# Performance work log

Hardware: AMD Instinct MI355X
Metric: run time of the kernel (lower is better)

The kernel has to match this reference:

```python
import jax, jax.numpy as jnp
import numpy as np

EPS = 1e-5  # torch GroupNorm default


def setup_inputs() -> dict:
    key = jax.random.key(0)
    ks = jax.random.split(key, 6)
    C = 256
    B, F, H, W = 1, 8, 32, 32
    scale = 1.0 / np.sqrt(C)  # keep logits well-scaled
    return {
        "x": jax.random.normal(ks[0], (B, C, F, H, W), dtype=jnp.float32),
        "gn_w": jnp.ones((C,), jnp.float32),
        "gn_b": jnp.zeros((C,), jnp.float32),
        "qw": jax.random.normal(ks[1], (C, C), jnp.float32) * scale,
        "qb": jnp.zeros((C,), jnp.float32),
        "kw": jax.random.normal(ks[2], (C, C), jnp.float32) * scale,
        "kb": jnp.zeros((C,), jnp.float32),
        "vw": jax.random.normal(ks[3], (C, C), jnp.float32) * scale,
        "vb": jnp.zeros((C,), jnp.float32),
        "ow": jax.random.normal(ks[4], (C, C), jnp.float32) * scale,
        "ob": jnp.zeros((C,), jnp.float32),
    }


def reference(x, gn_w, gn_b, qw, qb, kw, kb, vw, vb, ow, ob):
    B, C, F, H, W = x.shape
    N = F * H * W
    # GroupNorm(1, C): normalize over (C,F,H,W) per sample, per-channel affine
    mean = jnp.mean(x, axis=(1, 2, 3, 4), keepdims=True)
    var = jnp.var(x, axis=(1, 2, 3, 4), keepdims=True)
    xn = (x - mean) * jax.lax.rsqrt(var + EPS)
    xn = xn * gn_w[None, :, None, None, None] + gn_b[None, :, None, None, None]
    xf = xn.reshape(B, C, N)  # [B, C, N]
    # 1x1x1 Conv3d == channel matmul
    q = jnp.einsum('oc,bcn->bon', qw, xf) + qb[None, :, None]
    k = jnp.einsum('oc,bcn->bon', kw, xf) + kb[None, :, None]
    v = jnp.einsum('oc,bcn->bon', vw, xf) + vb[None, :, None]
    # scores[b, n_q, n_k] = q^T k, scaled by C^-0.5
    scores = jnp.einsum('bcn,bcm->bnm', q, k) * (C ** -0.5)
    weights = jax.nn.softmax(scores, axis=-1)  # over keys
    # attention[b, c, n_q] = sum_m v[b,c,m] * weights[b,n_q,m]
    att = jnp.einsum('bcm,bnm->bcn', v, weights)
    att = jnp.einsum('oc,bcn->bon', ow, att) + ob[None, :, None]
    return xn + att.reshape(B, C, F, H, W)
```

## Files before the change

kernel.cpp:

```cpp
#include <hip/hip_runtime.h>
#include <hip/hip_bf16.h>
#include <cstdint>

#define NSP 8192
#define CCH 256
#define KBLK 32
#define NSPLIT 8
#define KEYS_PER_SPLIT 1024
#define NTILES 32

typedef __attribute__((ext_vector_type(4))) float f32x4;
typedef __attribute__((ext_vector_type(16))) float f32x16;
typedef __attribute__((ext_vector_type(8))) short bf16x8;
typedef __attribute__((ext_vector_type(2))) unsigned int u32x2;

__device__ __forceinline__ ushort f2bf(float f) {
  union { float f; uint32_t u; } v; v.f = f;
  uint32_t r = (v.u + 0x7FFFu + ((v.u >> 16) & 1u)) >> 16;
  return (ushort)r;
}
__device__ __forceinline__ float bf2f(ushort u) {
  union { uint32_t u; float f; } v; v.u = ((uint32_t)u) << 16; return v.f;
}
__device__ __forceinline__ uint32_t pk2bf(float lo, float hi) {
  __hip_bfloat162 h = __float22bfloat162_rn({lo, hi});
  union { __hip_bfloat162 h; uint32_t u; } c; c.h = h; return c.u;
}

__device__ __forceinline__ void gload_lds16(const void* g, void* l) {
  auto gp = (const __attribute__((address_space(1))) uint32_t*)(uintptr_t)g;
  auto lp = (__attribute__((address_space(3))) uint32_t*)(uint32_t)(uintptr_t)l;
  __builtin_amdgcn_global_load_lds(gp, lp, 16, 0, 0);
}

__device__ __forceinline__ void perm32swap(uint32_t& a, uint32_t& b) {
#if __has_builtin(__builtin_amdgcn_permlane32_swap)
  u32x2 r = __builtin_amdgcn_permlane32_swap(a, b, false, false);
  a = r[0]; b = r[1];
#else
  uint32_t sa = __shfl_xor((int)a, 32), sb = __shfl_xor((int)b, 32);
  bool lo = (threadIdx.x & 63) < 32;
  uint32_t na = lo ? a : sb;
  uint32_t nb = lo ? sa : b;
  a = na; b = nb;
#endif
}

__global__ __launch_bounds__(256) void k_stats1(const float* __restrict__ x,
                                                float* __restrict__ part) {
  int t = threadIdx.x, b = blockIdx.x;
  float s = 0.f, ss = 0.f;
  const float4* x4 = (const float4*)x;
  for (int i = 0; i < 4; ++i) {
    float4 v = x4[(size_t)i * 131072 + b * 256 + t];
    s += v.x + v.y + v.z + v.w;
    ss += v.x * v.x + v.y * v.y + v.z * v.z + v.w * v.w;
  }
  for (int m = 1; m < 64; m <<= 1) { s += __shfl_xor(s, m); ss += __shfl_xor(ss, m); }
  __shared__ float ls[4], lss[4];
  int w = t >> 6, lane = t & 63;
  if (lane == 0) { ls[w] = s; lss[w] = ss; }
  __syncthreads();
  if (t == 0) {
    part[b * 2 + 0] = ls[0] + ls[1] + ls[2] + ls[3];
    part[b * 2 + 1] = lss[0] + lss[1] + lss[2] + lss[3];
  }
}

__global__ __launch_bounds__(256) void k_castw(const float* __restrict__ qw, const float* __restrict__ kw,
                                               const float* __restrict__ vw, const float* __restrict__ ow,
                                               ushort* __restrict__ wqkv, ushort* __restrict__ wo,
                                               const float* __restrict__ part, float* __restrict__ stat) {
  if (blockIdx.x == 1024) {
    int t = threadIdx.x;
    float s = 0.f, ss = 0.f;
    for (int i = t; i < 512; i += 256) { s += part[i * 2]; ss += part[i * 2 + 1]; }
    for (int m = 1; m < 64; m <<= 1) { s += __shfl_xor(s, m); ss += __shfl_xor(ss, m); }
    __shared__ float ls[4], lss[4];
    int w = t >> 6, lane = t & 63;
    if (lane == 0) { ls[w] = s; lss[w] = ss; }
    __syncthreads();
    if (t == 0) {
      float sum = ls[0] + ls[1] + ls[2] + ls[3];
      float ssum = lss[0] + lss[1] + lss[2] + lss[3];
      float mean = sum * (1.f / 2097152.f);
      float var = ssum * (1.f / 2097152.f) - mean * mean;
      stat[0] = mean;
      stat[1] = rsqrtf(var + 1e-5f);
    }
    return;
  }
  int idx = blockIdx.x * 256 + threadIdx.x;
  if (idx < 65536) wqkv[idx] = f2bf(qw[idx]);
  else if (idx < 131072) wqkv[idx] = f2bf(kw[idx - 65536]);
  else if (idx < 196608) wqkv[idx] = f2bf(vw[idx - 131072]);
  else wo[idx - 196608] = f2bf(ow[idx - 196608]);
}

__global__ __launch_bounds__(256) void k_norm_t(const float* __restrict__ x,
                                                const float* __restrict__ gw, const float* __restrict__ gb,
                                                const float* __restrict__ stat, ushort* __restrict__ xnT) {
  __shared__ float tile[64][66];
  int n0 = blockIdx.x * 64, c0 = blockIdx.y * 64;
  int t = threadIdx.x, colr = t & 63, rq = t >> 6;
  float mean = stat[0], rinv = stat[1];
  for (int rr = 0; rr < 16; ++rr) {
    int row = rr * 4 + rq;
    int c = c0 + row;
    float v = x[(size_t)c * NSP + n0 + colr];
    tile[row][colr] = (v - mean) * rinv * gw[c] + gb[c];
  }
  __syncthreads();
  for (int rr = 0; rr < 16; ++rr) {
    int rowW = rr * 4 + rq;
    xnT[(size_t)(n0 + rowW) * 256 + c0 + colr] = f2bf(tile[colr][rowW]);
  }
}

__global__ __launch_bounds__(256) void k_qkv(const ushort* __restrict__ xnT, const ushort* __restrict__ wqkv,
                                             const float* __restrict__ qb, const float* __restrict__ kb,
                                             const float* __restrict__ vb,
                                             ushort* __restrict__ qT, ushort* __restrict__ kT,
                                             ushort* __restrict__ v_cm) {
  __shared__ ushort tile[64][72];
  int nb = blockIdx.x, ob = blockIdx.y;
  int w = threadIdx.x >> 6, lane = threadIdx.x & 63;
  int l16 = lane & 15, kgrp = lane >> 4;
  int n_row = nb * 64 + w * 16 + l16;
  bf16x8 a[8];
  const bf16x8* arow = (const bf16x8*)(xnT + (size_t)n_row * 256);
  for (int ks = 0; ks < 8; ++ks) a[ks] = arow[ks * 4 + kgrp];
  f32x4 acc[4];
  for (int ct = 0; ct < 4; ++ct) {
    int o = ob * 64 + ct * 16 + l16;
    const bf16x8* brow = (const bf16x8*)(wqkv + (size_t)o * 256);
    f32x4 c = {0.f, 0.f, 0.f, 0.f};
    for (int ks = 0; ks < 8; ++ks)
      c = __builtin_amdgcn_mfma_f32_16x16x32_bf16(a[ks], brow[ks * 4 + kgrp], c, 0, 0, 0);
    acc[ct] = c;
  }
  const float SCALE = 0.0625f * 1.44269504088896340736f;
  if (ob < 8) {
    for (int ct = 0; ct < 4; ++ct) {
      int o = ob * 64 + ct * 16 + l16;
      for (int r = 0; r < 4; ++r) {
        int n = nb * 64 + w * 16 + kgrp * 4 + r;
        float v = acc[ct][r];
        if (o < 256) qT[(size_t)n * 256 + o] = f2bf((v + qb[o]) * SCALE);
        else kT[(size_t)n * 256 + (o - 256)] = f2bf(v + kb[o - 256]);
      }
    }
  } else {
    for (int ct = 0; ct < 4; ++ct) {
      int o_l = ct * 16 + l16;
      for (int r = 0; r < 4; ++r) {
        int n_l = w * 16 + kgrp * 4 + r;
        tile[o_l][n_l] = f2bf(acc[ct][r] + vb[(ob - 8) * 64 + o_l]);
      }
    }
    __syncthreads();
    int row = threadIdx.x >> 2, seg = threadIdx.x & 3;
    char* dst = (char*)v_cm + ((size_t)((ob - 8) * 64 + row)) * 16384 + (size_t)nb * 128 + seg * 32;
    const uint4* srcp = (const uint4*)&tile[row][seg * 16];
    ((uint4*)dst)[0] = srcp[0];
    ((uint4*)dst)[1] = srcp[1];
  }
}

__global__ __launch_bounds__(256, 2) void k_attn(const ushort* __restrict__ qT, const ushort* __restrict__ kT,
                                                 const ushort* __restrict__ v_cm,
                                                 ushort* __restrict__ Opart, float* __restrict__ mpart,
                                                 float* __restrict__ lpart) {
  __shared__ __align__(16) ushort SMEM[32768];
  ushort* k_lds = SMEM;
  ushort* v_lds = SMEM + 16384;

  int bid = blockIdx.x;
  int split = bid & 7, qblk = bid >> 3;
  int t = threadIdx.x, w = t >> 6, lane = t & 63;
  int l31 = lane & 31, lhi = lane >> 5, l7 = lane & 7;
  int q0w = qblk * 128 + w * 32;

  bf16x8 qf[16];
  {
    const char* qbase = (const char*)qT + (size_t)(q0w + l31) * 512;
#pragma unroll
    for (int cs = 0; cs < 16; ++cs)
      qf[cs] = *(const bf16x8*)(qbase + cs * 32 + lhi * 16);
  }

  f32x16 acc[8] = {};
  float m_r = -1e30f, l_p = 0.f;

  const char* kT_b = (const char*)kT + (size_t)split * KEYS_PER_SPLIT * 512;
  const char* v_b = (const char*)v_cm + (size_t)split * KEYS_PER_SPLIT * 2;

  auto STAGE = [&](int tt, int bsel) {
    const char* ksrc = kT_b + (size_t)tt * KBLK * 512;
    char* kdst = (char*)(k_lds + bsel * 8192) + w * 4096;
#pragma unroll
    for (int i = 0; i < 4; ++i) {
      int keyloc = w * 8 + i * 2 + lhi;
      int srcoff = keyloc * 512 + ((l31 ^ (keyloc & 7)) << 4);
      gload_lds16(ksrc + srcoff, kdst + i * 1024);
    }
    char* vdst = (char*)(v_lds + bsel * 8192) + w * 4096;
    const char* vsrc = v_b + (size_t)tt * 64 + w * 16;
#pragma unroll
    for (int i = 0; i < 4; ++i) {
      int c = i * 64 + lane;
      gload_lds16(vsrc + (size_t)c * 16384, vdst + i * 1024);
    }
  };

  STAGE(0, 0);

#pragma unroll 1
  for (int tt = 0; tt < NTILES; ++tt) {
    int cur = tt & 1;
    asm volatile("s_waitcnt vmcnt(0) lgkmcnt(0)" ::: "memory");
    __builtin_amdgcn_s_barrier();
    __builtin_amdgcn_sched_barrier(0);
    if (tt + 1 < NTILES) STAGE(tt + 1, cur ^ 1);

    const ushort* kl = k_lds + cur * 8192;
    f32x16 S0 = {};
    __builtin_amdgcn_s_setprio(1);
#pragma unroll
    for (int cs = 0; cs < 16; ++cs) {
      int slot = (cs * 2 + lhi) ^ l7;
      bf16x8 a0 = *(const bf16x8*)(kl + l31 * 256 + slot * 8);
      S0 = __builtin_amdgcn_mfma_f32_32x32x16_bf16(a0, qf[cs], S0, 0, 0, 0);
    }
    __builtin_amdgcn_s_setprio(0);

    float x0 = fmaxf(S0[0], S0[1]), x1 = fmaxf(S0[2], S0[3]);
    float x2 = fmaxf(S0[4], S0[5]), x3 = fmaxf(S0[6], S0[7]);
    float x4 = fmaxf(S0[8], S0[9]), x5 = fmaxf(S0[10], S0[11]);
    float x6 = fmaxf(S0[12], S0[13]), x7 = fmaxf(S0[14], S0[15]);
    float pm = fmaxf(fmaxf(fmaxf(x0, x1), fmaxf(x2, x3)),
                     fmaxf(fmaxf(x4, x5), fmaxf(x6, x7)));
    pm = fmaxf(pm, __shfl_xor(pm, 32));
    if (!__all(pm <= m_r + 8.f)) {
      float mn = fmaxf(m_r, pm);
      float alpha = __builtin_amdgcn_exp2f(m_r - mn);
      m_r = mn;
      l_p *= alpha;
#pragma unroll
      for (int cb = 0; cb < 8; ++cb)
#pragma unroll
        for (int r = 0; r < 16; ++r) acc[cb][r] *= alpha;
    }
    {
      float t0s = 0.f, t1s = 0.f, t2s = 0.f, t3s = 0.f;
#pragma unroll
      for (int r = 0; r < 16; ++r) {
        S0[r] = __builtin_amdgcn_exp2f(S0[r] - m_r);
        if (r < 4) t0s += S0[r];
        else if (r < 8) t1s += S0[r];
        else if (r < 12) t2s += S0[r];
        else t3s += S0[r];
      }
      l_p += (t0s + t1s) + (t2s + t3s);
    }

    bf16x8 pf[2];
    {
      union { uint32_t w[4]; bf16x8 v; } u;
#pragma unroll
      for (int h = 0; h < 2; ++h) {
        int b = h * 8;
        uint32_t x = pk2bf(S0[b + 0], S0[b + 1]), y = pk2bf(S0[b + 4], S0[b + 5]);
        perm32swap(x, y);
        uint32_t x2_ = pk2bf(S0[b + 2], S0[b + 3]), y2 = pk2bf(S0[b + 6], S0[b + 7]);
        perm32swap(x2_, y2);
        u.w[0] = x; u.w[1] = x2_; u.w[2] = y; u.w[3] = y2;
        pf[h] = u.v;
      }
    }

    const ushort* vl = v_lds + cur * 8192;
    __builtin_amdgcn_s_setprio(1);
#pragma unroll
    for (int cb = 0; cb < 8; ++cb) {
#pragma unroll
      for (int h = 0; h < 2; ++h) {
        int s = h * 2 + lhi;
        bf16x8 a = *(const bf16x8*)(vl + s * 2048 + (cb * 32 + l31) * 8);
        acc[cb] = __builtin_amdgcn_mfma_f32_32x32x16_bf16(a, pf[h], acc[cb], 0, 0, 0);
      }
    }
    __builtin_amdgcn_s_setprio(0);
  }

  asm volatile("s_waitcnt vmcnt(0) lgkmcnt(0)" ::: "memory");
  __builtin_amdgcn_s_barrier();

  float l_tot = l_p + __shfl_xor(l_p, 32);

  char* eb = (char*)SMEM + w * 8704;
  size_t gq0 = (size_t)split * NSP + q0w;
#pragma unroll
  for (int ch = 0; ch < 2; ++ch) {
#pragma unroll
    for (int cb4 = 0; cb4 < 4; ++cb4) {
      int cb = ch * 4 + cb4;
#pragma unroll
      for (int gsub = 0; gsub < 4; ++gsub) {
        int cl = cb4 * 32 + gsub * 8 + 4 * lhi;
        *(uint32_t*)(eb + l31 * 272 + cl * 2) = pk2bf(acc[cb][gsub * 4 + 0], acc[cb][gsub * 4 + 1]);
        *(uint32_t*)(eb + l31 * 272 + cl * 2 + 4) = pk2bf(acc[cb][gsub * 4 + 2], acc[cb][gsub * 4 + 3]);
      }
    }
#pragma unroll
    for (int i = 0; i < 8; ++i) {
      int flat = i * 1024 + lane * 16;
      int qr = flat >> 8, off = flat & 255;
      uint4 val = *(const uint4*)(eb + qr * 272 + off);
      *(uint4*)((char*)Opart + (gq0 + qr) * 512 + ch * 256 + off) = val;
    }
  }
  if (lane < 32) {
    int q = q0w + l31;
    mpart[split * NSP + q] = m_r;
    lpart[split * NSP + q] = l_tot;
  }
}

__global__ __launch_bounds__(256) void k_combine(const ushort* __restrict__ Opart,
                                                 const float* __restrict__ mpart,
                                                 const float* __restrict__ lpart,
                                                 ushort* __restrict__ attT) {
  int q = blockIdx.x;
  int c = threadIdx.x;
  float M = -1e30f;
  for (int s = 0; s < NSPLIT; ++s) M = fmaxf(M, mpart[s * NSP + q]);
  float L = 0.f, acc = 0.f;
  for (int s = 0; s < NSPLIT; ++s) {
    float ws = __builtin_amdgcn_exp2f(mpart[s * NSP + q] - M);
    L += ws * lpart[s * NSP + q];
    acc += ws * bf2f(Opart[((size_t)s * NSP + q) * 256 + c]);
  }
  attT[(size_t)q * 256 + c] = f2bf(acc / L);
}

__global__ __launch_bounds__(256) void k_final(const ushort* __restrict__ attT, const ushort* __restrict__ wo,
                                               const float* __restrict__ ob, const float* __restrict__ x,
                                               const float* __restrict__ gw, const float* __restrict__ gb,
                                               const float* __restrict__ stat, float* __restrict__ out) {
  int nb = blockIdx.x, obk = blockIdx.y;
  int w = threadIdx.x >> 6, lane = threadIdx.x & 63;
  int l16 = lane & 15, kgrp = lane >> 4;
  int orow = obk * 64 + w * 16 + l16;
  bf16x8 a[8];
  const bf16x8* arow = (const bf16x8*)(wo + (size_t)orow * 256);
  for (int ks = 0; ks < 8; ++ks) a[ks] = arow[ks * 4 + kgrp];
  float mean = stat[0], rinv = stat[1];
  f32x4 acc[4];
  for (int ct = 0; ct < 4; ++ct) {
    int n = nb * 64 + ct * 16 + l16;
    const bf16x8* brow = (const bf16x8*)(attT + (size_t)n * 256);
    f32x4 c = {0.f, 0.f, 0.f, 0.f};
    for (int ks = 0; ks < 8; ++ks)
      c = __builtin_amdgcn_mfma_f32_16x16x32_bf16(a[ks], brow[ks * 4 + kgrp], c, 0, 0, 0);
    acc[ct] = c;
  }
  for (int ct = 0; ct < 4; ++ct) {
    for (int r = 0; r < 4; ++r) {
      int o = obk * 64 + w * 16 + kgrp * 4 + r;
      int n = nb * 64 + ct * 16 + l16;
      float xv = x[(size_t)o * NSP + n];
      float xn = (xv - mean) * rinv * gw[o] + gb[o];
      out[(size_t)o * NSP + n] = xn + acc[ct][r] + ob[o];
    }
  }
}

extern "C" void kernel_launch(void* const* d_in, const int* in_sizes, int n_in,
                              void* d_out, int out_size, void* d_ws, size_t ws_size,
                              hipStream_t stream) {
  const float* x = (const float*)d_in[0];
  const float* gw = (const float*)d_in[1];
  const float* gb = (const float*)d_in[2];
  const float* qw = (const float*)d_in[3];
  const float* qbv = (const float*)d_in[4];
  const float* kw = (const float*)d_in[5];
  const float* kbv = (const float*)d_in[6];
  const float* vw = (const float*)d_in[7];
  const float* vbv = (const float*)d_in[8];
  const float* ow = (const float*)d_in[9];
  const float* obv = (const float*)d_in[10];
  float* out = (float*)d_out;
  char* ws = (char*)d_ws;
  const size_t KB = 1024, MB = 1048576;
  float* part = (float*)(ws);
  float* stat = (float*)(ws + 60 * KB);
  ushort* wqkv = (ushort*)(ws + 64 * KB);
  ushort* wo = (ushort*)(ws + 448 * KB);
  float* mpart = (float*)(ws + 64 * KB);
  float* lpart = (float*)(ws + 576 * KB);
  ushort* xnT = (ushort*)(ws + 1 * MB);
  ushort* qT = (ushort*)(ws + 5 * MB);
  ushort* kT = (ushort*)(ws + 9 * MB);
  ushort* v_cm = (ushort*)(ws + 13 * MB);
  ushort* Opart = (ushort*)(ws + 17 * MB);
  ushort* attT = xnT;

  k_stats1<<<512, 256, 0, stream>>>(x, part);
  k_castw<<<1025, 256, 0, stream>>>(qw, kw, vw, ow, wqkv, wo, part, stat);
  k_norm_t<<<dim3(128, 4), 256, 0, stream>>>(x, gw, gb, stat, xnT);
  k_qkv<<<dim3(128, 12), 256, 0, stream>>>(xnT, wqkv, qbv, kbv, vbv, qT, kT, v_cm);
  k_attn<<<512, 256, 0, stream>>>(qT, kT, v_cm, Opart, mpart, lpart);
  k_combine<<<NSP, 256, 0, stream>>>(Opart, mpart, lpart, attT);
  k_final<<<dim3(128, 4), 256, 0, stream>>>(attT, wo, obv, x, gw, gb, stat, out);
}
```

Measured before the change: 159.8 us.

## Double attention block to 8 waves and pre-tile V for contiguous staging

The attention kernel now runs 512-thread blocks covering 256 queries, so each staged K/V tile in LDS is shared by eight waves instead of four. This halves the global-to-LDS traffic per query. The QKV kernel now writes V directly in the per-tile, per-slot layout the attention kernel consumes, so staging becomes contiguous 16-byte loads instead of strided per-channel reads. The epilogue is reworked into smaller per-wave chunks so it fits the same LDS, at the risk of lower occupancy and register pressure from the larger block.

After: 145.6 us. 8.9% less time.

```diff
diff --git a/kernel.cpp b/kernel.cpp
--- a/kernel.cpp
+++ b/kernel.cpp
@@ -121,8 +121,8 @@
                                              const float* __restrict__ qb, const float* __restrict__ kb,
                                              const float* __restrict__ vb,
                                              ushort* __restrict__ qT, ushort* __restrict__ kT,
-                                             ushort* __restrict__ v_cm) {
-  __shared__ ushort tile[64][72];
+                                             ushort* __restrict__ v_tiles) {
+  __shared__ ushort tile[64][80];
   int nb = blockIdx.x, ob = blockIdx.y;
   int w = threadIdx.x >> 6, lane = threadIdx.x & 63;
   int l16 = lane & 15, kgrp = lane >> 4;
@@ -159,16 +159,18 @@
       }
     }
     __syncthreads();
-    int row = threadIdx.x >> 2, seg = threadIdx.x & 3;
-    char* dst = (char*)v_cm + ((size_t)((ob - 8) * 64 + row)) * 16384 + (size_t)nb * 128 + seg * 32;
-    const uint4* srcp = (const uint4*)&tile[row][seg * 16];
-    ((uint4*)dst)[0] = srcp[0];
-    ((uint4*)dst)[1] = srcp[1];
-  }
-}
-
-__global__ __launch_bounds__(256, 2) void k_attn(const ushort* __restrict__ qT, const ushort* __restrict__ kT,
-                                                 const ushort* __restrict__ v_cm,
+    for (int j = 0; j < 2; ++j) {
+      int idx = j * 256 + threadIdx.x;
+      int tile_l = idx >> 8, slot = (idx >> 6) & 3, c_l = idx & 63;
+      size_t off = (size_t)(nb * 2 + tile_l) * 8192 + slot * 2048 +
+                   (size_t)((ob - 8) * 64 + c_l) * 8;
+      *(uint4*)((char*)v_tiles + off * 2) = *(const uint4*)&tile[c_l][tile_l * 32 + slot * 8];
+    }
+  }
+}
+
+__global__ __launch_bounds__(512, 2) void k_attn(const ushort* __restrict__ qT, const ushort* __restrict__ kT,
+                                                 const ushort* __restrict__ v_tiles,
                                                  ushort* __restrict__ Opart, float* __restrict__ mpart,
                                                  float* __restrict__ lpart) {
   __shared__ __align__(16) ushort SMEM[32768];
@@ -179,7 +181,7 @@
   int split = bid & 7, qblk = bid >> 3;
   int t = threadIdx.x, w = t >> 6, lane = t & 63;
   int l31 = lane & 31, lhi = lane >> 5, l7 = lane & 7;
-  int q0w = qblk * 128 + w * 32;
+  int q0w = qblk * 256 + w * 32;
 
   bf16x8 qf[16];
   {
@@ -193,24 +195,22 @@
   float m_r = -1e30f, l_p = 0.f;
 
   const char* kT_b = (const char*)kT + (size_t)split * KEYS_PER_SPLIT * 512;
-  const char* v_b = (const char*)v_cm + (size_t)split * KEYS_PER_SPLIT * 2;
+  const char* v_b = (const char*)v_tiles + (size_t)split * KEYS_PER_SPLIT * 512;
 
   auto STAGE = [&](int tt, int bsel) {
     const char* ksrc = kT_b + (size_t)tt * KBLK * 512;
-    char* kdst = (char*)(k_lds + bsel * 8192) + w * 4096;
-#pragma unroll
-    for (int i = 0; i < 4; ++i) {
-      int keyloc = w * 8 + i * 2 + lhi;
+    char* kdst = (char*)(k_lds + bsel * 8192) + w * 2048;
+#pragma unroll
+    for (int i = 0; i < 2; ++i) {
+      int keyloc = w * 4 + i * 2 + lhi;
       int srcoff = keyloc * 512 + ((l31 ^ (keyloc & 7)) << 4);
       gload_lds16(ksrc + srcoff, kdst + i * 1024);
     }
-    char* vdst = (char*)(v_lds + bsel * 8192) + w * 4096;
-    const char* vsrc = v_b + (size_t)tt * 64 + w * 16;
-#pragma unroll
-    for (int i = 0; i < 4; ++i) {
-      int c = i * 64 + lane;
-      gload_lds16(vsrc + (size_t)c * 16384, vdst + i * 1024);
-    }
+    char* vdst = (char*)(v_lds + bsel * 8192) + w * 2048;
+    const char* vsrc = v_b + (size_t)tt * 16384 + w * 2048;
+#pragma unroll
+    for (int i = 0; i < 2; ++i)
+      gload_lds16(vsrc + i * 1024 + lane * 16, vdst + i * 1024);
   };
 
   STAGE(0, 0);
@@ -298,27 +298,31 @@
 
   float l_tot = l_p + __shfl_xor(l_p, 32);
 
-  char* eb = (char*)SMEM + w * 8704;
+  char* eb = (char*)SMEM + w * 4608;
   size_t gq0 = (size_t)split * NSP + q0w;
 #pragma unroll
-  for (int ch = 0; ch < 2; ++ch) {
-#pragma unroll
-    for (int cb4 = 0; cb4 < 4; ++cb4) {
-      int cb = ch * 4 + cb4;
-#pragma unroll
-      for (int gsub = 0; gsub < 4; ++gsub) {
-        int cl = cb4 * 32 + gsub * 8 + 4 * lhi;
-        *(uint32_t*)(eb + l31 * 272 + cl * 2) = pk2bf(acc[cb][gsub * 4 + 0], acc[cb][gsub * 4 + 1]);
-        *(uint32_t*)(eb + l31 * 272 + cl * 2 + 4) = pk2bf(acc[cb][gsub * 4 + 2], acc[cb][gsub * 4 + 3]);
-      }
-    }
-#pragma unroll
-    for (int i = 0; i < 8; ++i) {
+  for (int ch = 0; ch < 4; ++ch) {
+#pragma unroll
+    for (int cb2 = 0; cb2 < 2; ++cb2) {
+      int cb = ch * 2 + cb2;
+#pragma unroll
+      for (int g = 0; g < 4; ++g) {
+        int cl = cb2 * 32 + g * 8 + 4 * lhi;
+        *(uint32_t*)(eb + l31 * 144 + cl * 2) = pk2bf(acc[cb][g * 4 + 0], acc[cb][g * 4 + 1]);
+        *(uint32_t*)(eb + l31 * 144 + cl * 2 + 4) = pk2bf(acc[cb][g * 4 + 2], acc[cb][g * 4 + 3]);
+      }
+    }
+    asm volatile("s_waitcnt lgkmcnt(0)" ::: "memory");
+    __builtin_amdgcn_sched_barrier(0);
+#pragma unroll
+    for (int i = 0; i < 4; ++i) {
       int flat = i * 1024 + lane * 16;
-      int qr = flat >> 8, off = flat & 255;
-      uint4 val = *(const uint4*)(eb + qr * 272 + off);
-      *(uint4*)((char*)Opart + (gq0 + qr) * 512 + ch * 256 + off) = val;
-    }
+      int qr = flat >> 7, off = flat & 127;
+      uint4 val = *(const uint4*)(eb + qr * 144 + off);
+      *(uint4*)((char*)Opart + (gq0 + qr) * 512 + ch * 128 + off) = val;
+    }
+    asm volatile("s_waitcnt lgkmcnt(0)" ::: "memory");
+    __builtin_amdgcn_sched_barrier(0);
   }
   if (lane < 32) {
     int q = q0w + l31;
@@ -402,15 +406,15 @@
   ushort* xnT = (ushort*)(ws + 1 * MB);
   ushort* qT = (ushort*)(ws + 5 * MB);
   ushort* kT = (ushort*)(ws + 9 * MB);
-  ushort* v_cm = (ushort*)(ws + 13 * MB);
+  ushort* v_tiles = (ushort*)(ws + 13 * MB);
   ushort* Opart = (ushort*)(ws + 17 * MB);
   ushort* attT = xnT;
 
   k_stats1<<<512, 256, 0, stream>>>(x, part);
   k_castw<<<1025, 256, 0, stream>>>(qw, kw, vw, ow, wqkv, wo, part, stat);
   k_norm_t<<<dim3(128, 4), 256, 0, stream>>>(x, gw, gb, stat, xnT);
-  k_qkv<<<dim3(128, 12), 256, 0, stream>>>(xnT, wqkv, qbv, kbv, vbv, qT, kT, v_cm);
-  k_attn<<<512, 256, 0, stream>>>(qT, kT, v_cm, Opart, mpart, lpart);
+  k_qkv<<<dim3(128, 12), 256, 0, stream>>>(xnT, wqkv, qbv, kbv, vbv, qT, kT, v_tiles);
+  k_attn<<<256, 512, 0, stream>>>(qT, kT, v_tiles, Opart, mpart, lpart);
   k_combine<<<NSP, 256, 0, stream>>>(Opart, mpart, lpart, attT);
   k_final<<<dim3(128, 4), 256, 0, stream>>>(attT, wo, obv, x, gw, gb, stat, out);
 }
```
